# Performance work log

Hardware: AMD Instinct MI355X
Metric: run time of the kernel (lower is better)

Reference implementation:

```python
import jax, jax.numpy as jnp
import numpy as np

ND, NL, E, M = 8000, 16000, 60000, 50000  # disease nodes, lncrna nodes, edges, label edges
H = 16  # attention heads


def _gat(h_src, h_dst, src, dst, Ws, Wd, a_s, a_d, b, n_dst):
    # PyG GATConv: bipartite, concat heads, add_self_loops=False, negative_slope=0.2
    Hh, C = a_s.shape
    zs = (h_src @ Ws).reshape(-1, Hh, C)   # [Ns,H,C]
    zd = (h_dst @ Wd).reshape(-1, Hh, C)   # [Nd,H,C]
    al = (zs * a_s).sum(-1)[src] + (zd * a_d).sum(-1)[dst]  # [E,H]
    al = jax.nn.leaky_relu(al, negative_slope=0.2)
    m = jax.ops.segment_max(al, dst, num_segments=n_dst)
    m = jnp.where(jnp.isfinite(m), m, 0.0)  # guard empty segments
    e = jnp.exp(al - m[dst])
    s = jax.ops.segment_sum(e, dst, num_segments=n_dst)
    alpha = e / (s[dst] + 1e-16)            # softmax over incoming edges per dst
    msg = zs[src] * alpha[:, :, None]       # [E,H,C]
    out = jax.ops.segment_sum(msg, dst, num_segments=n_dst)
    return out.reshape(n_dst, Hh * C) + b


def _head_mean(x):
    x = jax.nn.relu(x)
    return x.reshape(x.shape[0], H, -1).mean(axis=1)


def _forward(x_d, x_l, emb_d, emb_l, lin_dw, lin_db, lin_lw, lin_lb,
             Wsrc1, Wdst1, asrc1, adst1, b1,
             Wsrc2, Wdst2, asrc2, adst2, b2,
             Wsrc3, Wdst3, asrc3, adst3, b3,
             pw, pb, fc1w, fc1b, fc2w, fc2b,
             node_id_d, node_id_l, edge_src, edge_dst, label_src, label_dst):
    hd = x_d @ lin_dw + lin_db + emb_d[node_id_d]   # [ND,128]
    hl = x_l @ lin_lw + lin_lb + emb_l[node_id_l]   # [NL,128]
    for (Ws, Wd, a_s, a_d, b) in ((Wsrc1, Wdst1, asrc1, adst1, b1),
                                  (Wsrc2, Wdst2, asrc2, adst2, b2),
                                  (Wsrc3, Wdst3, asrc3, adst3, b3)):
        # to_hetero: edge-type 0 = disease->lncrna (target lncrna); 1 = reverse
        out_l = _gat(hd, hl, edge_src, edge_dst, Ws[0], Wd[0], a_s[0], a_d[0], b[0], NL)
        out_d = _gat(hl, hd, edge_dst, edge_src, Ws[1], Wd[1], a_s[1], a_d[1], b[1], ND)
        hd, hl = _head_mean(out_d), _head_mean(out_l)
    # penalty scaling (per node type after to_hetero); transformer branch is dead code
    hd = hd * jnp.exp(hd @ pw[0] + pb[0])
    hl = hl * jnp.exp(hl @ pw[1] + pb[1])
    f = jnp.concatenate([hd[label_src], hl[label_dst]], axis=-1)  # [M,64]
    return jax.nn.relu(f @ fc1w + fc1b) @ fc2w + fc2b              # [M,1]


def setup_inputs():
    key = jax.random.key(0)
    ks = jax.random.split(key, 40)
    def rn(i, shape, scale=1.0):
        return jax.random.normal(ks[i], shape, dtype=jnp.float32) * scale
    return dict(
        x_d=rn(0, (ND, 412)), x_l=rn(1, (NL, 240)),
        node_id_d=jnp.arange(ND), node_id_l=jnp.arange(NL),
        edge_src=jax.random.randint(ks[2], (E,), 0, ND),
        edge_dst=jax.random.randint(ks[3], (E,), 0, NL),
        label_src=jax.random.randint(ks[4], (M,), 0, ND),
        label_dst=jax.random.randint(ks[5], (M,), 0, NL),
        emb_d=rn(6, (ND, 128), 0.1), emb_l=rn(7, (NL, 128), 0.1),
        lin_dw=rn(8, (412, 128), 412 ** -0.5), lin_db=rn(9, (128,), 0.02),
        lin_lw=rn(10, (240, 128), 240 ** -0.5), lin_lb=rn(11, (128,), 0.02),
        Wsrc1=rn(12, (2, 128, 2048), 128 ** -0.5), Wdst1=rn(13, (2, 128, 2048), 128 ** -0.5),
        asrc1=rn(14, (2, H, 128), 0.05), adst1=rn(15, (2, H, 128), 0.05), b1=rn(16, (2, 2048), 0.02),
        Wsrc2=rn(17, (2, 128, 2048), 128 ** -0.5), Wdst2=rn(18, (2, 128, 2048), 128 ** -0.5),
        asrc2=rn(19, (2, H, 128), 0.05), adst2=rn(20, (2, H, 128), 0.05), b2=rn(21, (2, 2048), 0.02),
        Wsrc3=rn(22, (2, 128, 512), 128 ** -0.5), Wdst3=rn(23, (2, 128, 512), 128 ** -0.5),
        asrc3=rn(24, (2, H, 32), 0.05), adst3=rn(25, (2, H, 32), 0.05), b3=rn(26, (2, 512), 0.02),
        pw=rn(27, (2, 32, 1), 0.05), pb=rn(28, (2, 1), 0.01),
        fc1w=rn(29, (64, 64), 64 ** -0.5), fc1b=rn(30, (64,), 0.02),
        fc2w=rn(31, (64, 1), 64 ** -0.5), fc2b=rn(32, (1,), 0.02),
    )


def reference(x_d, x_l, node_id_d, node_id_l, edge_src, edge_dst, label_src, label_dst,
              emb_d, emb_l, lin_dw, lin_db, lin_lw, lin_lb,
              Wsrc1, Wdst1, asrc1, adst1, b1,
              Wsrc2, Wdst2, asrc2, adst2, b2,
              Wsrc3, Wdst3, asrc3, adst3, b3,
              pw, pb, fc1w, fc1b, fc2w, fc2b):
    return _forward(x_d, x_l, emb_d, emb_l, lin_dw, lin_db, lin_lw, lin_lb,
                    Wsrc1, Wdst1, asrc1, adst1, b1,
                    Wsrc2, Wdst2, asrc2, adst2, b2,
                    Wsrc3, Wdst3, asrc3, adst3, b3,
                    pw, pb, fc1w, fc1b, fc2w, fc2b,
                    node_id_d, node_id_l, edge_src, edge_dst, label_src, label_dst)
```

## Files before the change

kernel.cpp:

```cpp
#include <hip/hip_runtime.h>
#include <cstdint>
#include <cstddef>

#define ND 8000
#define NL 16000
#define NE 60000
#define NM 50000

typedef __attribute__((ext_vector_type(8))) short bf16x8;
typedef __attribute__((ext_vector_type(4))) float f32x4;
typedef __attribute__((ext_vector_type(8))) unsigned int u32x8;

__device__ __forceinline__ unsigned short f2bf(float x) {
    unsigned int u = __float_as_uint(x);
    unsigned int r = (u + 0x7FFFu + ((u >> 16) & 1u)) >> 16;
    return (unsigned short)r;
}
__device__ __forceinline__ float bf2f(unsigned short b) {
    return __uint_as_float(((unsigned int)b) << 16);
}
__device__ __forceinline__ float lrelu(float x) {
    return x >= 0.f ? x : 0.2f * x;
}

__device__ __forceinline__ void gl_lds16(const void* g, void* l) {
    __builtin_amdgcn_global_load_lds(
        (const __attribute__((address_space(1))) void*)g,
        (__attribute__((address_space(3))) void*)l, 16, 0, 0);
}

__global__ void wtin_kernel(const float* __restrict__ Wd, const float* __restrict__ Wl,
                            unsigned short* __restrict__ WinH, unsigned short* __restrict__ WinL)
{
    int gid = blockIdx.x * 256 + threadIdx.x;
    if (gid >= 53248 + 32768) return;
    const float* W; int K, KC; unsigned short* oH; unsigned short* oL; int rem;
    if (gid < 53248) { W = Wd; K = 412; KC = 13; rem = gid; oH = WinH; oL = WinL; }
    else { W = Wl; K = 240; KC = 8; rem = gid - 53248; oH = WinH + 53248; oL = WinL + 53248; }
    int k = rem >> 7, n = rem & 127;
    float v = (k < K) ? W[(size_t)k * 128 + n] : 0.f;
    unsigned short hb = f2bf(v);
    unsigned short lb = f2bf(v - bf2f(hb));
    int u = n >> 4;
    int kc = k >> 5;
    int lane = (n & 15) + 16 * ((k >> 3) & 3);
    size_t o = ((size_t)u * KC + kc) * 512 + lane * 8 + (k & 7);
    oH[o] = hb;
    oL[o] = lb;
}

__global__ __launch_bounds__(256) void inlinm_kernel(
    const float* __restrict__ x_d, const float* __restrict__ x_l,
    const unsigned short* __restrict__ WinH, const unsigned short* __restrict__ WinL,
    const float* __restrict__ bd, const float* __restrict__ bl,
    const float* __restrict__ embd, const float* __restrict__ embl,
    const int* __restrict__ nidd, const int* __restrict__ nidl,
    float* __restrict__ hd, float* __restrict__ hl)
{
    const int tid = threadIdx.x;
    const int wave = tid >> 6;
    const int lane = tid & 63;
    const int i = blockIdx.x;
    const int cb = i & 1;
    int mt = i >> 1;
    const float* X; int K, KC;
    const unsigned short* wH; const unsigned short* wL;
    const float* bias; const float* emb; const int* nid; float* out;
    if (mt < 125) {
        X = x_d; K = 412; KC = 13; wH = WinH; wL = WinL;
        bias = bd; emb = embd; nid = nidd; out = hd;
    } else {
        mt -= 125;
        X = x_l; K = 240; KC = 8; wH = WinH + 53248; wL = WinL + 53248;
        bias = bl; emb = embl; nid = nidl; out = hl;
    }
    const int m0 = mt * 64 + wave * 16;
    const int row = lane & 15;
    const int quad = lane >> 4;

    f32x4 accH[4] = {};
    f32x4 accL[4] = {};

    const float* xr = X + (size_t)(m0 + row) * K;
    for (int kc = 0; kc < KC; ++kc) {
        int k0 = kc * 32 + quad * 8;
        float xv[8];
        if (k0 + 8 <= K) {
            float4 v0 = *(const float4*)(xr + k0);
            float4 v1 = *(const float4*)(xr + k0 + 4);
            xv[0] = v0.x; xv[1] = v0.y; xv[2] = v0.z; xv[3] = v0.w;
            xv[4] = v1.x; xv[5] = v1.y; xv[6] = v1.z; xv[7] = v1.w;
        } else {
#pragma unroll
            for (int j = 0; j < 8; ++j)
                xv[j] = (k0 + j < K) ? xr[k0 + j] : 0.f;
        }
        bf16x8 aH, aL;
#pragma unroll
        for (int j = 0; j < 8; ++j) {
            unsigned short hb = f2bf(xv[j]);
            aH[j] = (short)hb;
            aL[j] = (short)f2bf(xv[j] - bf2f(hb));
        }
#pragma unroll
        for (int u = 0; u < 4; ++u) {
            int ug = cb * 4 + u;
            size_t boff = ((size_t)ug * KC + kc) * 512 + lane * 8;
            bf16x8 bH = *(const bf16x8*)(wH + boff);
            bf16x8 bL = *(const bf16x8*)(wL + boff);
            accH[u] = __builtin_amdgcn_mfma_f32_16x16x32_bf16(aH, bH, accH[u], 0, 0, 0);
            accL[u] = __builtin_amdgcn_mfma_f32_16x16x32_bf16(aH, bL, accL[u], 0, 0, 0);
            accL[u] = __builtin_amdgcn_mfma_f32_16x16x32_bf16(aL, bH, accL[u], 0, 0, 0);
        }
    }
#pragma unroll
    for (int r = 0; r < 4; ++r) {
        int gm = m0 + quad * 4 + r;
        const float* ep = emb + (size_t)nid[gm] * 128;
        float* op = out + (size_t)gm * 128;
#pragma unroll
        for (int u = 0; u < 4; ++u) {
            int gn = (cb * 4 + u) * 16 + row;
            op[gn] = accH[u][r] + accL[u][r] + bias[gn] + ep[gn];
        }
    }
}

__global__ void wt2_kernel(const float* __restrict__ W0, const float* __restrict__ W1,
                           unsigned short* __restrict__ WtH, unsigned short* __restrict__ WtL)
{
    int gid = blockIdx.x * 256 + threadIdx.x;
    if (gid >= 2 * 2 * 128 * 2048) return;
    int l = gid >> 19;
    int rem0 = gid & 524287;
    int dir = rem0 >> 18;
    int rem = rem0 & 262143;
    int k = rem >> 11, n = rem & 2047;
    const float* W = l ? W1 : W0;
    float v = W[(size_t)dir * 262144 + (size_t)k * 2048 + n];
    unsigned short hb = f2bf(v);
    unsigned short lb = f2bf(v - bf2f(hb));
    int u = n >> 4;
    int lane = (n & 15) + 16 * ((k >> 3) & 3);
    size_t o = (size_t)l * 524288 + (size_t)dir * 262144 +
               ((size_t)u * 4 + (k >> 5)) * 512 + lane * 8 + (k & 7);
    WtH[o] = hb;
    WtL[o] = lb;
}

__global__ void wt3_kernel(const float* __restrict__ W3,
                           unsigned short* __restrict__ WtH3, unsigned short* __restrict__ WtL3)
{
    int gid = blockIdx.x * 256 + threadIdx.x;
    if (gid >= 2 * 128 * 512) return;
    int dir = gid >> 16;
    int rem = gid & 65535;
    int k = rem >> 9, n = rem & 511;
    float v = W3[(size_t)dir * 65536 + (size_t)k * 512 + n];
    unsigned short hb = f2bf(v);
    unsigned short lb = f2bf(v - bf2f(hb));
    int u = n >> 4;
    int lane = (n & 15) + 16 * ((k >> 3) & 3);
    size_t o = (size_t)dir * 65536 + ((size_t)u * 4 + (k >> 5)) * 512 + lane * 8 + (k & 7);
    WtH3[o] = hb;
    WtL3[o] = lb;
}

__global__ void pack3_kernel(const float* __restrict__ hd, const float* __restrict__ hl,
                             unsigned int* __restrict__ pAd, unsigned int* __restrict__ pAl)
{
    int gid = blockIdx.x * 256 + threadIdx.x;
    if (gid >= (ND + NL) * 128) return;
    int row = gid >> 7, k = gid & 127;
    const float* src; unsigned int* dst; int gm;
    if (row < ND) { src = hd; dst = pAd; gm = row; }
    else { src = hl; dst = pAl; gm = row - ND; }
    float v = src[(size_t)gm * 128 + k];
    unsigned short hb = f2bf(v);
    unsigned short lb = f2bf(v - bf2f(hb));
    int t = gm >> 4;
    int lane8 = ((gm & 15) + 16 * ((k >> 3) & 3)) * 8 + (k & 7);
    size_t idx = ((size_t)t * 4 + (k >> 5)) * 512 + lane8;
    dst[idx] = (unsigned int)hb | ((unsigned int)lb << 16);
}

__global__ __launch_bounds__(256) void gemm3m_kernel(
    const unsigned int* __restrict__ pAd, const unsigned int* __restrict__ pAl,
    const unsigned short* __restrict__ WtH3, const unsigned short* __restrict__ WtL3,
    float* __restrict__ zs3d, float* __restrict__ zs3l)
{
    const int tid = threadIdx.x;
    const int wave = tid >> 6;
    const int lane = tid & 63;
    const int cb = blockIdx.x & 1;
    int mt = blockIdx.x >> 1;
    const unsigned int* pA_; const unsigned short* wH; const unsigned short* wL; float* zs;
    if (mt < 125) { pA_ = pAd; wH = WtH3; wL = WtL3; zs = zs3d; }
    else { mt -= 125; pA_ = pAl; wH = WtH3 + 65536; wL = WtL3 + 65536; zs = zs3l; }
    const int m0 = mt * 64 + wave * 16;
    const int t = m0 >> 4;
    const int row = lane & 15;
    const int quad = lane >> 4;

    bf16x8 aH[4], aL[4];
#pragma unroll
    for (int kc = 0; kc < 4; ++kc) {
        u32x8 p = *(const u32x8*)(pA_ + ((size_t)t * 4 + kc) * 512 + lane * 8);
#pragma unroll
        for (int ii = 0; ii < 8; ++ii) {
            aH[kc][ii] = (short)(p[ii] & 0xffffu);
            aL[kc][ii] = (short)(p[ii] >> 16);
        }
    }

#pragma unroll 2
    for (int u = 0; u < 16; ++u) {
        const int ug = cb * 16 + u;
        f32x4 accH = (f32x4){0.f, 0.f, 0.f, 0.f};
        f32x4 accL = (f32x4){0.f, 0.f, 0.f, 0.f};
#pragma unroll
        for (int kc = 0; kc < 4; ++kc) {
            size_t boff = ((size_t)ug * 4 + kc) * 512 + lane * 8;
            bf16x8 bH = *(const bf16x8*)(wH + boff);
            bf16x8 bL = *(const bf16x8*)(wL + boff);
            accH = __builtin_amdgcn_mfma_f32_16x16x32_bf16(aH[kc], bH, accH, 0, 0, 0);
            accL = __builtin_amdgcn_mfma_f32_16x16x32_bf16(aH[kc], bL, accL, 0, 0, 0);
            accL = __builtin_amdgcn_mfma_f32_16x16x32_bf16(aL[kc], bH, accL, 0, 0, 0);
        }
        const int gn = ug * 16 + row;
#pragma unroll
        for (int r = 0; r < 4; ++r) {
            int gm = m0 + quad * 4 + r;
            zs[(size_t)gm * 512 + gn] = accH[r] + accL[r];
        }
    }
}

__global__ __launch_bounds__(256) void gemm2r_kernel(
    const unsigned int* __restrict__ haggPl, const unsigned int* __restrict__ haggPd,
    const unsigned short* __restrict__ WtHb, const unsigned short* __restrict__ WtLb,
    const float* __restrict__ biasb, float* __restrict__ outl, float* __restrict__ outd)
{
    __shared__ unsigned short BsH[2][4096];
    __shared__ unsigned short BsL[2][4096];

    const int tid = threadIdx.x;
    const int wave = tid >> 6;
    const int lane = tid & 63;
    const int bid = blockIdx.x;

    const unsigned int* haggP; const unsigned short* wHb; const unsigned short* wLb;
    const float* bias; float* out;
    int mt, cb, nmt;
    if (bid < 1024) {
        int g = bid & 7, rest = bid >> 3;
        mt = (rest >> 2) * 8 + g; cb = rest & 3; nmt = 250;
        haggP = haggPl; wHb = WtHb; wLb = WtLb; bias = biasb; out = outl;
    } else {
        int b2 = bid - 1024;
        int g = b2 & 7, rest = b2 >> 3;
        mt = (rest >> 2) * 8 + g; cb = rest & 3; nmt = 125;
        haggP = haggPd; wHb = WtHb + 262144; wLb = WtLb + 262144;
        bias = biasb + 2048; out = outd;
    }
    if (mt >= nmt) return;

    const int m0 = mt * 64 + wave * 16;
    const int t = m0 >> 4;
    const int row = lane & 15;
    const int quad = lane >> 4;

    const unsigned short* gHb = wHb + (size_t)cb * 4096;
    const unsigned short* gLb = wLb + (size_t)cb * 4096;

    u32x8 pA[4];
    f32x4 mean[2] = {};

#pragma unroll
    for (int j = 0; j < 2; ++j) {
        int o = (tid + j * 256) * 16;
        gl_lds16((const char*)gHb + o, (char*)&BsH[0][0] + o);
        gl_lds16((const char*)gLb + o, (char*)&BsL[0][0] + o);
    }
#pragma unroll
    for (int kc = 0; kc < 4; ++kc)
        pA[kc] = *(const u32x8*)(haggP + (((size_t)t * 16 + 0) * 4 + kc) * 512 + lane * 8);
    __syncthreads();

    int buf = 0;
    for (int h = 0; h < 16; ++h) {
        bf16x8 aH[4], aL[4];
#pragma unroll
        for (int kc = 0; kc < 4; ++kc) {
#pragma unroll
            for (int ii = 0; ii < 8; ++ii) {
                aH[kc][ii] = (short)(pA[kc][ii] & 0xffffu);
                aL[kc][ii] = (short)(pA[kc][ii] >> 16);
            }
        }
        if (h < 15) {
            const char* gH = (const char*)(gHb + (size_t)(h + 1) * 16384);
            const char* gL = (const char*)(gLb + (size_t)(h + 1) * 16384);
            char* lH = (char*)&BsH[buf ^ 1][0];
            char* lL = (char*)&BsL[buf ^ 1][0];
#pragma unroll
            for (int j = 0; j < 2; ++j) {
                int o = (tid + j * 256) * 16;
                gl_lds16(gH + o, lH + o);
                gl_lds16(gL + o, lL + o);
            }
#pragma unroll
            for (int kc = 0; kc < 4; ++kc)
                pA[kc] = *(const u32x8*)(haggP + (((size_t)t * 16 + h + 1) * 4 + kc) * 512 + lane * 8);
        }

#pragma unroll
        for (int ctl = 0; ctl < 2; ++ctl) {
            float bv = bias[h * 128 + cb * 32 + ctl * 16 + row];
            f32x4 accH = (f32x4){bv, bv, bv, bv};
            f32x4 accL = (f32x4){0.f, 0.f, 0.f, 0.f};
#pragma unroll
            for (int kc = 0; kc < 4; ++kc) {
                bf16x8 bH = *(const bf16x8*)&BsH[buf][(ctl * 4 + kc) * 512 + lane * 8];
                bf16x8 bL = *(const bf16x8*)&BsL[buf][(ctl * 4 + kc) * 512 + lane * 8];
                accH = __builtin_amdgcn_mfma_f32_16x16x32_bf16(aH[kc], bH, accH, 0, 0, 0);
                accL = __builtin_amdgcn_mfma_f32_16x16x32_bf16(aH[kc], bL, accL, 0, 0, 0);
                accL = __builtin_amdgcn_mfma_f32_16x16x32_bf16(aL[kc], bH, accL, 0, 0, 0);
            }
#pragma unroll
            for (int r = 0; r < 4; ++r)
                mean[ctl][r] += fmaxf(accH[r] + accL[r], 0.f);
        }
        __syncthreads();
        buf ^= 1;
    }

#pragma unroll
    for (int ctl = 0; ctl < 2; ++ctl) {
        int c = cb * 32 + ctl * 16 + row;
#pragma unroll
        for (int r = 0; r < 4; ++r) {
            int gm = m0 + quad * 4 + r;
            out[(size_t)gm * 128 + c] = mean[ctl][r] * (1.f / 16.f);
        }
    }
}

__global__ void fold3_kernel(
    const float* __restrict__ Ws1, const float* __restrict__ Wd1,
    const float* __restrict__ as1, const float* __restrict__ ad1,
    const float* __restrict__ Ws2, const float* __restrict__ Wd2,
    const float* __restrict__ as2, const float* __restrict__ ad2,
    const float* __restrict__ Ws3, const float* __restrict__ Wd3,
    const float* __restrict__ as3, const float* __restrict__ ad3,
    float* __restrict__ fw3)
{
    int gid = blockIdx.x * blockDim.x + threadIdx.x;
    if (gid >= 3 * 4 * 128 * 16) return;
    int l = gid / 8192, rem1 = gid % 8192;
    int f = rem1 / 2048, rem = rem1 % 2048;
    int k = rem >> 4, h = rem & 15;
    int Ntot = (l == 2) ? 512 : 2048;
    int C = Ntot >> 4;
    const float* W;
    const float* a;
    if (l == 0) { W = (f & 1) ? Wd1 : Ws1; a = (f & 1) ? ad1 : as1; }
    else if (l == 1) { W = (f & 1) ? Wd2 : Ws2; a = (f & 1) ? ad2 : as2; }
    else { W = (f & 1) ? Wd3 : Ws3; a = (f & 1) ? ad3 : as3; }
    if (f >= 2) { W += 128 * Ntot; a += 16 * C; }
    float s = 0.f;
    for (int c = 0; c < C; ++c) s += W[(size_t)k * Ntot + h * C + c] * a[h * C + c];
    fw3[gid] = s;
}

__global__ __launch_bounds__(256) void score2both_kernel(
    const float* __restrict__ Hd, const float* __restrict__ Hl,
    const float* __restrict__ fw,
    float* __restrict__ ssb0, float* __restrict__ sdb1,
    float* __restrict__ sdb0, float* __restrict__ ssb1)
{
    __shared__ float hs[16 * 128];
    __shared__ float wa[128 * 16];
    __shared__ float wb[128 * 16];
    int b = blockIdx.x;
    const float* Hf; const float* WfA; const float* WfB;
    float* outA; float* outB; int n0;
    if (b < ND / 16) {
        Hf = Hd; WfA = fw; WfB = fw + 3 * 2048; outA = ssb0; outB = sdb1; n0 = b * 16;
    } else {
        Hf = Hl; WfA = fw + 1 * 2048; WfB = fw + 2 * 2048; outA = sdb0; outB = ssb1;
        n0 = (b - ND / 16) * 16;
    }
    int tid = threadIdx.x;
#pragma unroll
    for (int i = 0; i < 8; ++i) {
        int idx = tid + i * 256;
        int nl = idx >> 7, k = idx & 127;
        hs[idx] = Hf[(size_t)(n0 + nl) * 128 + k];
        wa[idx] = WfA[idx];
        wb[idx] = WfB[idx];
    }
    __syncthreads();
    int nl = tid >> 4, h = tid & 15;
    float sa = 0.f, sb = 0.f;
    for (int k = 0; k < 128; ++k) {
        float hv = hs[nl * 128 + k];
        sa += hv * wa[k * 16 + h];
        sb += hv * wb[k * 16 + h];
    }
    int gn = n0 + nl;
    outA[gn * 16 + h] = sa;
    outB[gn * 16 + h] = sb;
}

__global__ void ms_kernel(
    const int* __restrict__ esrc, const int* __restrict__ edst,
    const float* __restrict__ ssb0, const float* __restrict__ sdb0,
    const float* __restrict__ ssb1, const float* __restrict__ sdb1,
    const int* __restrict__ offl, const int* __restrict__ csrl, float* __restrict__ msl,
    const int* __restrict__ offd, const int* __restrict__ csrd, float* __restrict__ msd)
{
    int t = blockIdx.x * 256 + threadIdx.x;
    const int* off; const int* csr; const int* srcidx;
    const float* ss; float sdv; float* ms; int d, h;
    if (t < NL * 16) {
        d = t >> 4; h = t & 15;
        off = offl; csr = csrl; srcidx = esrc; ss = ssb0;
        sdv = sdb0[d * 16 + h]; ms = msl;
    } else {
        t -= NL * 16;
        if (t >= ND * 16) return;
        d = t >> 4; h = t & 15;
        off = offd; csr = csrd; srcidx = edst; ss = ssb1;
        sdv = sdb1[d * 16 + h]; ms = msd;
    }
    int e0 = off[d], e1 = off[d + 1];
    float m = -1e30f, s = 0.f;
    for (int e = e0; e < e1; ++e) {
        int sn = srcidx[csr[e]];
        float a = lrelu(ss[sn * 16 + h] + sdv);
        if (a > m) { s = s * __expf(m - a) + 1.f; m = a; }
        else s += __expf(a - m);
    }
    ms[d * 32 + h] = m;
    ms[d * 32 + 16 + h] = s + 1e-16f;
}

__global__ void hist_kernel(const int* __restrict__ esrc, const int* __restrict__ edst,
                            int* __restrict__ degl, int* __restrict__ degd)
{
    int e = blockIdx.x * blockDim.x + threadIdx.x;
    if (e >= NE) return;
    atomicAdd(&degl[edst[e]], 1);
    atomicAdd(&degd[esrc[e]], 1);
}

__global__ __launch_bounds__(1024) void scan2_kernel(
    const int* __restrict__ degA, int* __restrict__ offA, int nA,
    const int* __restrict__ degB, int* __restrict__ offB, int nB)
{
    __shared__ int ps[1024];
    const int* deg = blockIdx.x ? degB : degA;
    int* off = blockIdx.x ? offB : offA;
    int n = blockIdx.x ? nB : nA;
    int tid = threadIdx.x;
    int chunk = (n + 1023) >> 10;
    int start = tid * chunk, end = min(start + chunk, n);
    int p = 0;
    for (int i = start; i < end; ++i) p += deg[i];
    ps[tid] = p;
    __syncthreads();
    for (int o = 1; o < 1024; o <<= 1) {
        int v = (tid >= o) ? ps[tid - o] : 0;
        __syncthreads();
        ps[tid] += v;
        __syncthreads();
    }
    int run = ps[tid] - p;
    for (int i = start; i < end; ++i) { off[i] = run; run += deg[i]; }
    if (tid == 1023) off[n] = ps[1023];
}

__global__ void scatter_kernel(const int* __restrict__ esrc, const int* __restrict__ edst,
                               const int* __restrict__ offl, const int* __restrict__ offd,
                               int* __restrict__ curl, int* __restrict__ curd,
                               int* __restrict__ csrl, int* __restrict__ csrd)
{
    int e = blockIdx.x * blockDim.x + threadIdx.x;
    if (e >= NE) return;
    int dl = edst[e]; int p = atomicAdd(&curl[dl], 1); csrl[offl[dl] + p] = e;
    int dd = esrc[e]; int q = atomicAdd(&curd[dd], 1); csrd[offd[dd] + q] = e;
}

__global__ __launch_bounds__(256) void hagg2_kernel(
    const float* __restrict__ hd, const float* __restrict__ hl,
    const float* __restrict__ ssb0, const float* __restrict__ sdb0, const float* __restrict__ msl,
    const float* __restrict__ ssb1, const float* __restrict__ sdb1, const float* __restrict__ msd,
    const int* __restrict__ offl, const int* __restrict__ csrl,
    const int* __restrict__ offd, const int* __restrict__ csrd,
    const int* __restrict__ esrc, const int* __restrict__ edst,
    unsigned int* __restrict__ haggPl, unsigned int* __restrict__ haggPd)
{
    __shared__ float alpha_s[2][8][17];
    __shared__ int src_s[2][8];
    const int b = blockIdx.x;
    const int tid = threadIdx.x;

    const float* hsrc; const float* ss; const float* sd; const float* ms;
    const int* off; const int* csr; const int* srcidx; unsigned int* haggP;
    int d0;
    if (b < NL / 2) {
        d0 = b * 2;
        hsrc = hd; ss = ssb0; sd = sdb0; ms = msl;
        off = offl; csr = csrl; srcidx = esrc; haggP = haggPl;
    } else {
        d0 = (b - NL / 2) * 2;
        hsrc = hl; ss = ssb1; sd = sdb1; ms = msd;
        off = offd; csr = csrd; srcidx = edst; haggP = haggPd;
    }

    const int half = tid >> 7;
    const int c = tid & 127;
    const int d = d0 + half;
    const int my_e0 = off[d];
    const int my_deg = off[d + 1] - my_e0;
    const int deg0 = off[d0 + 1] - off[d0];
    const int deg1 = off[d0 + 2] - off[d0 + 1];
    const int degmax = deg0 > deg1 ? deg0 : deg1;
    const int ntrip = (degmax + 7) >> 3;

    float acc[16];
#pragma unroll
    for (int h = 0; h < 16; ++h) acc[h] = 0.f;

    for (int trip = 0; trip < ntrip; ++trip) {
        int ce = trip * 8;
        {
            int ei = c >> 4, h = c & 15;
            if (ce + ei < my_deg) {
                int eid = csr[my_e0 + ce + ei];
                int sn = srcidx[eid];
                float a = lrelu(ss[sn * 16 + h] + sd[d * 16 + h]);
                alpha_s[half][ei][h] = __expf(a - ms[d * 32 + h]) / ms[d * 32 + 16 + h];
                if (h == 0) src_s[half][ei] = sn;
            }
        }
        __syncthreads();
        int nc = min(8, my_deg - ce);
        for (int ei = 0; ei < nc; ++ei) {
            float v = hsrc[(size_t)src_s[half][ei] * 128 + c];
#pragma unroll
            for (int h = 0; h < 16; ++h)
                acc[h] += alpha_s[half][ei][h] * v;
        }
        __syncthreads();
    }

    const int t = d >> 4;
    const int lane8 = ((d & 15) + 16 * ((c >> 3) & 3)) * 8 + (c & 7);
    const int kc = c >> 5;
#pragma unroll
    for (int h = 0; h < 16; ++h) {
        float v = acc[h];
        unsigned short hb = f2bf(v);
        unsigned short lb = f2bf(v - bf2f(hb));
        size_t idx = (((size_t)t * 16 + h) * 4 + kc) * 512 + lane8;
        haggP[idx] = (unsigned int)hb | ((unsigned int)lb << 16);
    }
}

__global__ __launch_bounds__(256) void agg32both_kernel(
    const float* __restrict__ zs3d, const float* __restrict__ zs3l,
    const float* __restrict__ ssb0, const float* __restrict__ sdb0, const float* __restrict__ msl,
    const float* __restrict__ ssb1, const float* __restrict__ sdb1, const float* __restrict__ msd,
    const int* __restrict__ offl, const int* __restrict__ csrl,
    const int* __restrict__ offd, const int* __restrict__ csrd,
    const int* __restrict__ esrc, const int* __restrict__ edst,
    const float* __restrict__ bias512,
    const float* __restrict__ pw, const float* __restrict__ pb,
    float* __restrict__ hlp, float* __restrict__ hdp)
{
    int d = blockIdx.x * 4 + (threadIdx.x >> 6);
    if (d >= NL + ND) return;
    const int lane = threadIdx.x & 63;

    const float* zs; const float* ss; const float* sd; const float* ms;
    const int* off; const int* csr; const int* srcidx;
    const float* bias; const float* pwt; const float* pbt; float* out;
    if (d < NL) {
        zs = zs3d; ss = ssb0; sd = sdb0; ms = msl;
        off = offl; csr = csrl; srcidx = esrc;
        bias = bias512; pwt = pw + 32; pbt = pb + 1; out = hlp;
    } else {
        d -= NL;
        zs = zs3l; ss = ssb1; sd = sdb1; ms = msd;
        off = offd; csr = csrd; srcidx = edst;
        bias = bias512 + 512; pwt = pw; pbt = pb; out = hdp;
    }

    const int h = lane >> 2;
    const int c0 = lane * 8;

    const float sdv = sd[d * 16 + h];
    const float mh = ms[d * 32 + h];
    const float sh = ms[d * 32 + 16 + h];
    const int e0 = off[d], e1 = off[d + 1];

    float acc[8] = {};
    for (int e = e0; e < e1; ++e) {
        int sn = srcidx[csr[e]];
        float a = lrelu(ss[sn * 16 + h] + sdv);
        float alpha = __expf(a - mh) / sh;
        const float* zr = zs + (size_t)sn * 512 + c0;
        float4 v0 = *(const float4*)zr;
        float4 v1 = *(const float4*)(zr + 4);
        acc[0] += alpha * v0.x; acc[1] += alpha * v0.y;
        acc[2] += alpha * v0.z; acc[3] += alpha * v0.w;
        acc[4] += alpha * v1.x; acc[5] += alpha * v1.y;
        acc[6] += alpha * v1.z; acc[7] += alpha * v1.w;
    }

#pragma unroll
    for (int i = 0; i < 8; ++i)
        acc[i] = fmaxf(acc[i] + bias[c0 + i], 0.f);

#pragma unroll
    for (int m = 4; m <= 32; m <<= 1)
#pragma unroll
        for (int i = 0; i < 8; ++i)
            acc[i] += __shfl_xor(acc[i], m);

    float hr[8];
#pragma unroll
    for (int i = 0; i < 8; ++i) hr[i] = acc[i] * (1.f / 16.f);

    float p = 0.f;
    const int ko = (lane & 3) * 8;
#pragma unroll
    for (int i = 0; i < 8; ++i) p += hr[i] * pwt[ko + i];
    p += __shfl_xor(p, 1);
    p += __shfl_xor(p, 2);
    float t = expf(p + pbt[0]);

    if (lane < 4) {
        float* op = out + (size_t)d * 32 + lane * 8;
#pragma unroll
        for (int i = 0; i < 8; ++i) op[i] = hr[i] * t;
    }
}

__global__ __launch_bounds__(256) void mlp_kernel(
    const float* __restrict__ hd, const float* __restrict__ hl,
    const int* __restrict__ ls, const int* __restrict__ ld,
    const float* __restrict__ w1, const float* __restrict__ b1,
    const float* __restrict__ w2, const float* __restrict__ b2,
    float* __restrict__ out, int M)
{
    __shared__ float w1s[64 * 64];
    __shared__ float b1s[64];
    __shared__ float w2s[64];
    int tid = threadIdx.x;
#pragma unroll
    for (int i = 0; i < 16; ++i) w1s[tid + i * 256] = w1[tid + i * 256];
    if (tid < 64) { b1s[tid] = b1[tid]; w2s[tid] = w2[tid]; }
    __syncthreads();
    int m = blockIdx.x * 256 + tid;
    if (m >= M) return;
    float f[64];
    const float* hp = hd + (size_t)ls[m] * 32;
    const float* lp = hl + (size_t)ld[m] * 32;
#pragma unroll
    for (int c = 0; c < 32; ++c) { f[c] = hp[c]; f[32 + c] = lp[c]; }
    float o = b2[0];
    for (int j = 0; j < 64; ++j) {
        float hj = b1s[j];
#pragma unroll
        for (int k = 0; k < 64; ++k) hj += f[k] * w1s[k * 64 + j];
        hj = fmaxf(hj, 0.f);
        o += hj * w2s[j];
    }
    out[m] = o;
}

extern "C" void kernel_launch(void* const* d_in, const int* in_sizes, int n_in,
                              void* d_out, int out_size, void* d_ws, size_t ws_size,
                              hipStream_t stream)
{
    const float* x_d = (const float*)d_in[0];
    const float* x_l = (const float*)d_in[1];
    const int* node_id_d = (const int*)d_in[2];
    const int* node_id_l = (const int*)d_in[3];
    const int* edge_src = (const int*)d_in[4];
    const int* edge_dst = (const int*)d_in[5];
    const int* label_src = (const int*)d_in[6];
    const int* label_dst = (const int*)d_in[7];
    const float* emb_d = (const float*)d_in[8];
    const float* emb_l = (const float*)d_in[9];
    const float* lin_dw = (const float*)d_in[10];
    const float* lin_db = (const float*)d_in[11];
    const float* lin_lw = (const float*)d_in[12];
    const float* lin_lb = (const float*)d_in[13];
    const float* Ws[3] = {(const float*)d_in[14], (const float*)d_in[19], (const float*)d_in[24]};
    const float* Wd[3] = {(const float*)d_in[15], (const float*)d_in[20], (const float*)d_in[25]};
    const float* as_[3] = {(const float*)d_in[16], (const float*)d_in[21], (const float*)d_in[26]};
    const float* ad_[3] = {(const float*)d_in[17], (const float*)d_in[22], (const float*)d_in[27]};
    const float* bb[3] = {(const float*)d_in[18], (const float*)d_in[23], (const float*)d_in[28]};
    const float* pw = (const float*)d_in[29];
    const float* pb = (const float*)d_in[30];
    const float* fc1w = (const float*)d_in[31];
    const float* fc1b = (const float*)d_in[32];
    const float* fc2w = (const float*)d_in[33];
    const float* fc2b = (const float*)d_in[34];

    char* wsb = (char*)d_ws;
    size_t woff = 0;
    auto carve = [&](size_t bytes) -> void* {
        woff = (woff + 255) & ~(size_t)255;
        void* p = wsb + woff;
        woff += bytes;
        return p;
    };
    float* hdA = (float*)carve((size_t)ND * 128 * 4);
    float* hlA = (float*)carve((size_t)NL * 128 * 4);
    float* hdB = (float*)carve((size_t)ND * 128 * 4);
    float* hlB = (float*)carve((size_t)NL * 128 * 4);
    unsigned int* haggPl = (unsigned int*)carve((size_t)NL * 2048 * 4);
    unsigned int* haggPd = (unsigned int*)carve((size_t)ND * 2048 * 4);
    unsigned short* WtH = (unsigned short*)carve((size_t)2 * 2 * 2048 * 128 * 2);
    unsigned short* WtL = (unsigned short*)carve((size_t)2 * 2 * 2048 * 128 * 2);
    unsigned short* WtH3 = (unsigned short*)carve((size_t)2 * 128 * 512 * 2);
    unsigned short* WtL3 = (unsigned short*)carve((size_t)2 * 128 * 512 * 2);
    unsigned short* WtInH = (unsigned short*)carve((size_t)(53248 + 32768) * 2);
    unsigned short* WtInL = (unsigned short*)carve((size_t)(53248 + 32768) * 2);
    unsigned int* pAd = (unsigned int*)carve((size_t)(ND / 16) * 4 * 512 * 4);
    unsigned int* pAl = (unsigned int*)carve((size_t)(NL / 16) * 4 * 512 * 4);
    float* ssb0 = (float*)carve((size_t)ND * 16 * 4);
    float* sdb0 = (float*)carve((size_t)NL * 16 * 4);
    float* ssb1 = (float*)carve((size_t)NL * 16 * 4);
    float* sdb1 = (float*)carve((size_t)ND * 16 * 4);
    float* msl = (float*)carve((size_t)NL * 32 * 4);
    float* msd = (float*)carve((size_t)ND * 32 * 4);
    float* fw3 = (float*)carve((size_t)3 * 4 * 2048 * 4);
    int* degl = (int*)carve((size_t)(2 * (NL + ND)) * 4);
    int* degd = degl + NL;
    int* curl = degd + ND;
    int* curd = curl + NL;
    int* offl = (int*)carve((size_t)(NL + 1) * 4);
    int* offd = (int*)carve((size_t)(ND + 1) * 4);
    int* csrl = (int*)carve((size_t)NE * 4);
    int* csrd = (int*)carve((size_t)NE * 4);
    float* hdp = (float*)carve((size_t)ND * 32 * 4);
    float* hlp = (float*)carve((size_t)NL * 32 * 4);

    hipMemsetAsync(degl, 0, (size_t)2 * (NL + ND) * 4, stream);

    hist_kernel<<<(NE + 255) / 256, 256, 0, stream>>>(edge_src, edge_dst, degl, degd);
    scan2_kernel<<<2, 1024, 0, stream>>>(degl, offl, NL, degd, offd, ND);
    scatter_kernel<<<(NE + 255) / 256, 256, 0, stream>>>(edge_src, edge_dst, offl, offd, curl, curd, csrl, csrd);

    fold3_kernel<<<(3 * 8192 + 255) / 256, 256, 0, stream>>>(
        Ws[0], Wd[0], as_[0], ad_[0], Ws[1], Wd[1], as_[1], ad_[1],
        Ws[2], Wd[2], as_[2], ad_[2], fw3);
    wt2_kernel<<<(2 * 524288 + 255) / 256, 256, 0, stream>>>(Ws[0], Ws[1], WtH, WtL);
    wt3_kernel<<<(2 * 65536 + 255) / 256, 256, 0, stream>>>(Ws[2], WtH3, WtL3);
    wtin_kernel<<<(53248 + 32768 + 255) / 256, 256, 0, stream>>>(lin_dw, lin_lw, WtInH, WtInL);

    inlinm_kernel<<<(125 + 250) * 2, 256, 0, stream>>>(
        x_d, x_l, WtInH, WtInL, lin_db, lin_lb, emb_d, emb_l,
        node_id_d, node_id_l, hdA, hlA);

    float* hd_cur = hdA; float* hd_nxt = hdB;
    float* hl_cur = hlA; float* hl_nxt = hlB;

    const int grid_ms = ((NL + ND) * 16 + 255) / 256;

    for (int L = 0; L < 2; ++L) {
        const float* fw = fw3 + (size_t)L * 8192;
        const unsigned short* wtH = WtH + (size_t)L * 524288;
        const unsigned short* wtL = WtL + (size_t)L * 524288;

        score2both_kernel<<<ND / 16 + NL / 16, 256, 0, stream>>>(
            hd_cur, hl_cur, fw, ssb0, sdb1, sdb0, ssb1);
        ms_kernel<<<grid_ms, 256, 0, stream>>>(edge_src, edge_dst, ssb0, sdb0, ssb1, sdb1,
                                               offl, csrl, msl, offd, csrd, msd);

        hagg2_kernel<<<NL / 2 + ND / 2, 256, 0, stream>>>(
            hd_cur, hl_cur, ssb0, sdb0, msl, ssb1, sdb1, msd,
            offl, csrl, offd, csrd, edge_src, edge_dst, haggPl, haggPd);

        gemm2r_kernel<<<1536, 256, 0, stream>>>(
            haggPl, haggPd, wtH, wtL, bb[L], hl_nxt, hd_nxt);

        float* t;
        t = hd_cur; hd_cur = hd_nxt; hd_nxt = t;
        t = hl_cur; hl_cur = hl_nxt; hl_nxt = t;
    }

    {
        const float* fw = fw3 + 2 * 8192;
        float* zs3d = (float*)haggPl;
        float* zs3l = (float*)haggPl + (size_t)ND * 512;
        score2both_kernel<<<ND / 16 + NL / 16, 256, 0, stream>>>(
            hd_cur, hl_cur, fw, ssb0, sdb1, sdb0, ssb1);
        ms_kernel<<<grid_ms, 256, 0, stream>>>(edge_src, edge_dst, ssb0, sdb0, ssb1, sdb1,
                                               offl, csrl, msl, offd, csrd, msd);

        pack3_kernel<<<((ND + NL) * 128 + 255) / 256, 256, 0, stream>>>(
            hd_cur, hl_cur, pAd, pAl);
        gemm3m_kernel<<<(125 + 250) * 2, 256, 0, stream>>>(
            pAd, pAl, WtH3, WtL3, zs3d, zs3l);

        agg32both_kernel<<<(NL + ND + 3) / 4, 256, 0, stream>>>(
            zs3d, zs3l, ssb0, sdb0, msl, ssb1, sdb1, msd,
            offl, csrl, offd, csrd, edge_src, edge_dst,
            bb[2], pw, pb, hlp, hdp);
    }

    mlp_kernel<<<(NM + 255) / 256, 256, 0, stream>>>(hdp, hlp, label_src, label_dst,
                                                     fc1w, fc1b, fc2w, fc2b, (float*)d_out, NM);
}
```

Before: 636.5 us.

## Restructure gemm2r to stage activations in LDS and stream weights from global

Result: no change. 625.8 us, median of 2 (-1.7%).

```diff
diff --git a/kernel.cpp b/kernel.cpp
--- a/kernel.cpp
+++ b/kernel.cpp
@@ -241,8 +241,7 @@
     const unsigned short* __restrict__ WtHb, const unsigned short* __restrict__ WtLb,
     const float* __restrict__ biasb, float* __restrict__ outl, float* __restrict__ outd)
 {
-    __shared__ unsigned short BsH[2][4096];
-    __shared__ unsigned short BsL[2][4096];
+    __shared__ unsigned int As[2][4096];
 
     const int tid = threadIdx.x;
     const int wave = tid >> 6;
@@ -250,100 +249,93 @@
     const int bid = blockIdx.x;
 
     const unsigned int* haggP; const unsigned short* wHb; const unsigned short* wLb;
-    const float* bias; float* out;
-    int mt, cb, nmt;
-    if (bid < 1024) {
-        int g = bid & 7, rest = bid >> 3;
-        mt = (rest >> 2) * 8 + g; cb = rest & 3; nmt = 250;
-        haggP = haggPl; wHb = WtHb; wLb = WtLb; bias = biasb; out = outl;
+    const float* bias; float* out; int mt;
+    if (bid < 500) {
+        mt = bid; haggP = haggPl; wHb = WtHb; wLb = WtLb; bias = biasb; out = outl;
     } else {
-        int b2 = bid - 1024;
-        int g = b2 & 7, rest = b2 >> 3;
-        mt = (rest >> 2) * 8 + g; cb = rest & 3; nmt = 125;
-        haggP = haggPd; wHb = WtHb + 262144; wLb = WtLb + 262144;
+        mt = bid - 500; haggP = haggPd; wHb = WtHb + 262144; wLb = WtLb + 262144;
         bias = biasb + 2048; out = outd;
     }
-    if (mt >= nmt) return;
-
-    const int m0 = mt * 64 + wave * 16;
-    const int t = m0 >> 4;
+    const int cb = wave;
+    const int t0 = mt * 2;
     const int row = lane & 15;
     const int quad = lane >> 4;
 
-    const unsigned short* gHb = wHb + (size_t)cb * 4096;
-    const unsigned short* gLb = wLb + (size_t)cb * 4096;
-
-    u32x8 pA[4];
-    f32x4 mean[2] = {};
-
-#pragma unroll
-    for (int j = 0; j < 2; ++j) {
-        int o = (tid + j * 256) * 16;
-        gl_lds16((const char*)gHb + o, (char*)&BsH[0][0] + o);
-        gl_lds16((const char*)gLb + o, (char*)&BsL[0][0] + o);
-    }
-#pragma unroll
-    for (int kc = 0; kc < 4; ++kc)
-        pA[kc] = *(const u32x8*)(haggP + (((size_t)t * 16 + 0) * 4 + kc) * 512 + lane * 8);
+    auto stageA = [&](int h, int b) {
+#pragma unroll
+        for (int j = 0; j < 4; ++j) {
+            int slot = tid + j * 256;
+            int t = slot >> 9;
+            const char* g = (const char*)(haggP + ((size_t)(t0 + t) * 16 + h) * 2048)
+                            + (size_t)(slot & 511) * 16;
+            char* l = (char*)&As[b][0] + (size_t)slot * 16;
+            gl_lds16(g, l);
+        }
+    };
+
+    f32x4 mean[2][2] = {};
+
+    stageA(0, 0);
     __syncthreads();
 
     int buf = 0;
     for (int h = 0; h < 16; ++h) {
-        bf16x8 aH[4], aL[4];
-#pragma unroll
-        for (int kc = 0; kc < 4; ++kc) {
-#pragma unroll
-            for (int ii = 0; ii < 8; ++ii) {
-                aH[kc][ii] = (short)(pA[kc][ii] & 0xffffu);
-                aL[kc][ii] = (short)(pA[kc][ii] >> 16);
+        if (h < 15) stageA(h + 1, buf ^ 1);
+
+        bf16x8 aH[2][4], aL[2][4];
+#pragma unroll
+        for (int t = 0; t < 2; ++t)
+#pragma unroll
+            for (int kc = 0; kc < 4; ++kc) {
+                u32x8 p = *(const u32x8*)&As[buf][t * 2048 + kc * 512 + lane * 8];
+#pragma unroll
+                for (int ii = 0; ii < 8; ++ii) {
+                    aH[t][kc][ii] = (short)(p[ii] & 0xffffu);
+                    aL[t][kc][ii] = (short)(p[ii] >> 16);
+                }
             }
-        }
-        if (h < 15) {
-            const char* gH = (const char*)(gHb + (size_t)(h + 1) * 16384);
-            const char* gL = (const char*)(gLb + (size_t)(h + 1) * 16384);
-            char* lH = (char*)&BsH[buf ^ 1][0];
-            char* lL = (char*)&BsL[buf ^ 1][0];
-#pragma unroll
-            for (int j = 0; j < 2; ++j) {
-                int o = (tid + j * 256) * 16;
-                gl_lds16(gH + o, lH + o);
-                gl_lds16(gL + o, lL + o);
+
+#pragma unroll
+        for (int ctl = 0; ctl < 2; ++ctl) {
+            const int u = h * 8 + cb * 2 + ctl;
+            float bv = bias[h * 128 + cb * 32 + ctl * 16 + row];
+            f32x4 accH0 = (f32x4){bv, bv, bv, bv};
+            f32x4 accL0 = (f32x4){0.f, 0.f, 0.f, 0.f};
+            f32x4 accH1 = (f32x4){bv, bv, bv, bv};
+            f32x4 accL1 = (f32x4){0.f, 0.f, 0.f, 0.f};
+#pragma unroll
+            for (int kc = 0; kc < 4; ++kc) {
+                size_t boff = ((size_t)u * 4 + kc) * 512 + lane * 8;
+                bf16x8 bH = *(const bf16x8*)(wHb + boff);
+                bf16x8 bL = *(const bf16x8*)(wLb + boff);
+                accH0 = __builtin_amdgcn_mfma_f32_16x16x32_bf16(aH[0][kc], bH, accH0, 0, 0, 0);
+                accL0 = __builtin_amdgcn_mfma_f32_16x16x32_bf16(aH[0][kc], bL, accL0, 0, 0, 0);
+                accL0 = __builtin_amdgcn_mfma_f32_16x16x32_bf16(aL[0][kc], bH, accL0, 0, 0, 0);
+                accH1 = __builtin_amdgcn_mfma_f32_16x16x32_bf16(aH[1][kc], bH, accH1, 0, 0, 0);
+                accL1 = __builtin_amdgcn_mfma_f32_16x16x32_bf16(aH[1][kc], bL, accL1, 0, 0, 0);
+                accL1 = __builtin_amdgcn_mfma_f32_16x16x32_bf16(aL[1][kc], bH, accL1, 0, 0, 0);
             }
 #pragma unroll
-            for (int kc = 0; kc < 4; ++kc)
-                pA[kc] = *(const u32x8*)(haggP + (((size_t)t * 16 + h + 1) * 4 + kc) * 512 + lane * 8);
-        }
-
-#pragma unroll
-        for (int ctl = 0; ctl < 2; ++ctl) {
-            float bv = bias[h * 128 + cb * 32 + ctl * 16 + row];
-            f32x4 accH = (f32x4){bv, bv, bv, bv};
-            f32x4 accL = (f32x4){0.f, 0.f, 0.f, 0.f};
-#pragma unroll
-            for (int kc = 0; kc < 4; ++kc) {
-                bf16x8 bH = *(const bf16x8*)&BsH[buf][(ctl * 4 + kc) * 512 + lane * 8];
-                bf16x8 bL = *(const bf16x8*)&BsL[buf][(ctl * 4 + kc) * 512 + lane * 8];
-                accH = __builtin_amdgcn_mfma_f32_16x16x32_bf16(aH[kc], bH, accH, 0, 0, 0);
-                accL = __builtin_amdgcn_mfma_f32_16x16x32_bf16(aH[kc], bL, accL, 0, 0, 0);
-                accL = __builtin_amdgcn_mfma_f32_16x16x32_bf16(aL[kc], bH, accL, 0, 0, 0);
+            for (int r = 0; r < 4; ++r) {
+                mean[0][ctl][r] += fmaxf(accH0[r] + accL0[r], 0.f);
+                mean[1][ctl][r] += fmaxf(accH1[r] + accL1[r], 0.f);
             }
-#pragma unroll
-            for (int r = 0; r < 4; ++r)
-                mean[ctl][r] += fmaxf(accH[r] + accL[r], 0.f);
         }
         __syncthreads();
         buf ^= 1;
     }
 
 #pragma unroll
-    for (int ctl = 0; ctl < 2; ++ctl) {
-        int c = cb * 32 + ctl * 16 + row;
-#pragma unroll
-        for (int r = 0; r < 4; ++r) {
-            int gm = m0 + quad * 4 + r;
-            out[(size_t)gm * 128 + c] = mean[ctl][r] * (1.f / 16.f);
-        }
-    }
+    for (int t = 0; t < 2; ++t)
+#pragma unroll
+        for (int ctl = 0; ctl < 2; ++ctl) {
+            int c = cb * 32 + ctl * 16 + row;
+#pragma unroll
+            for (int r = 0; r < 4; ++r) {
+                int gm = mt * 32 + t * 16 + quad * 4 + r;
+                out[(size_t)gm * 128 + c] = mean[t][ctl][r] * (1.f / 16.f);
+            }
+        }
 }
 
 __global__ void fold3_kernel(
@@ -788,7 +780,7 @@
             hd_cur, hl_cur, ssb0, sdb0, msl, ssb1, sdb1, msd,
             offl, csrl, offd, csrd, edge_src, edge_dst, haggPl, haggPd);
 
-        gemm2r_kernel<<<1536, 256, 0, stream>>>(
+        gemm2r_kernel<<<500 + 250, 256, 0, stream>>>(
             haggPl, haggPd, wtH, wtL, bb[L], hl_nxt, hd_nxt);
 
         float* t;
```

## Drop LDS staging in gemm2r; each wave computes independent 16-row by 64-col tile

Applied to the files above, without the earlier changes.

Measured after the change: 669.7 us. 5.2% more time.

```diff
diff --git a/kernel.cpp b/kernel.cpp
--- a/kernel.cpp
+++ b/kernel.cpp
@@ -21,12 +21,6 @@
 }
 __device__ __forceinline__ float lrelu(float x) {
     return x >= 0.f ? x : 0.2f * x;
-}
-
-__device__ __forceinline__ void gl_lds16(const void* g, void* l) {
-    __builtin_amdgcn_global_load_lds(
-        (const __attribute__((address_space(1))) void*)g,
-        (__attribute__((address_space(3))) void*)l, 16, 0, 0);
 }
 
 __global__ void wtin_kernel(const float* __restrict__ Wd, const float* __restrict__ Wl,
@@ -241,53 +235,32 @@
     const unsigned short* __restrict__ WtHb, const unsigned short* __restrict__ WtLb,
     const float* __restrict__ biasb, float* __restrict__ outl, float* __restrict__ outd)
 {
-    __shared__ unsigned short BsH[2][4096];
-    __shared__ unsigned short BsL[2][4096];
-
     const int tid = threadIdx.x;
     const int wave = tid >> 6;
     const int lane = tid & 63;
-    const int bid = blockIdx.x;
+    int item = blockIdx.x * 4 + wave;
 
     const unsigned int* haggP; const unsigned short* wHb; const unsigned short* wLb;
-    const float* bias; float* out;
-    int mt, cb, nmt;
-    if (bid < 1024) {
-        int g = bid & 7, rest = bid >> 3;
-        mt = (rest >> 2) * 8 + g; cb = rest & 3; nmt = 250;
+    const float* bias; float* out; int t, cb;
+    if (item < 2000) {
+        t = item >> 1; cb = item & 1;
         haggP = haggPl; wHb = WtHb; wLb = WtLb; bias = biasb; out = outl;
     } else {
-        int b2 = bid - 1024;
-        int g = b2 & 7, rest = b2 >> 3;
-        mt = (rest >> 2) * 8 + g; cb = rest & 3; nmt = 125;
+        item -= 2000;
+        t = item >> 1; cb = item & 1;
         haggP = haggPd; wHb = WtHb + 262144; wLb = WtLb + 262144;
         bias = biasb + 2048; out = outd;
     }
-    if (mt >= nmt) return;
-
-    const int m0 = mt * 64 + wave * 16;
-    const int t = m0 >> 4;
     const int row = lane & 15;
     const int quad = lane >> 4;
 
-    const unsigned short* gHb = wHb + (size_t)cb * 4096;
-    const unsigned short* gLb = wLb + (size_t)cb * 4096;
-
     u32x8 pA[4];
-    f32x4 mean[2] = {};
-
-#pragma unroll
-    for (int j = 0; j < 2; ++j) {
-        int o = (tid + j * 256) * 16;
-        gl_lds16((const char*)gHb + o, (char*)&BsH[0][0] + o);
-        gl_lds16((const char*)gLb + o, (char*)&BsL[0][0] + o);
-    }
 #pragma unroll
     for (int kc = 0; kc < 4; ++kc)
         pA[kc] = *(const u32x8*)(haggP + (((size_t)t * 16 + 0) * 4 + kc) * 512 + lane * 8);
-    __syncthreads();
-
-    int buf = 0;
+
+    f32x4 mean[4] = {};
+
     for (int h = 0; h < 16; ++h) {
         bf16x8 aH[4], aL[4];
 #pragma unroll
@@ -299,30 +272,22 @@
             }
         }
         if (h < 15) {
-            const char* gH = (const char*)(gHb + (size_t)(h + 1) * 16384);
-            const char* gL = (const char*)(gLb + (size_t)(h + 1) * 16384);
-            char* lH = (char*)&BsH[buf ^ 1][0];
-            char* lL = (char*)&BsL[buf ^ 1][0];
-#pragma unroll
-            for (int j = 0; j < 2; ++j) {
-                int o = (tid + j * 256) * 16;
-                gl_lds16(gH + o, lH + o);
-                gl_lds16(gL + o, lL + o);
-            }
 #pragma unroll
             for (int kc = 0; kc < 4; ++kc)
                 pA[kc] = *(const u32x8*)(haggP + (((size_t)t * 16 + h + 1) * 4 + kc) * 512 + lane * 8);
         }
 
 #pragma unroll
-        for (int ctl = 0; ctl < 2; ++ctl) {
-            float bv = bias[h * 128 + cb * 32 + ctl * 16 + row];
+        for (int ctl = 0; ctl < 4; ++ctl) {
+            const int u = h * 8 + cb * 4 + ctl;
+            float bv = bias[h * 128 + cb * 64 + ctl * 16 + row];
             f32x4 accH = (f32x4){bv, bv, bv, bv};
             f32x4 accL = (f32x4){0.f, 0.f, 0.f, 0.f};
 #pragma unroll
             for (int kc = 0; kc < 4; ++kc) {
-                bf16x8 bH = *(const bf16x8*)&BsH[buf][(ctl * 4 + kc) * 512 + lane * 8];
-                bf16x8 bL = *(const bf16x8*)&BsL[buf][(ctl * 4 + kc) * 512 + lane * 8];
+                size_t boff = ((size_t)u * 4 + kc) * 512 + lane * 8;
+                bf16x8 bH = *(const bf16x8*)(wHb + boff);
+                bf16x8 bL = *(const bf16x8*)(wLb + boff);
                 accH = __builtin_amdgcn_mfma_f32_16x16x32_bf16(aH[kc], bH, accH, 0, 0, 0);
                 accL = __builtin_amdgcn_mfma_f32_16x16x32_bf16(aH[kc], bL, accL, 0, 0, 0);
                 accL = __builtin_amdgcn_mfma_f32_16x16x32_bf16(aL[kc], bH, accL, 0, 0, 0);
@@ -331,16 +296,14 @@
             for (int r = 0; r < 4; ++r)
                 mean[ctl][r] += fmaxf(accH[r] + accL[r], 0.f);
         }
-        __syncthreads();
-        buf ^= 1;
-    }
-
-#pragma unroll
-    for (int ctl = 0; ctl < 2; ++ctl) {
-        int c = cb * 32 + ctl * 16 + row;
+    }
+
+#pragma unroll
+    for (int ctl = 0; ctl < 4; ++ctl) {
+        int c = cb * 64 + ctl * 16 + row;
 #pragma unroll
         for (int r = 0; r < 4; ++r) {
-            int gm = m0 + quad * 4 + r;
+            int gm = t * 16 + quad * 4 + r;
             out[(size_t)gm * 128 + c] = mean[ctl][r] * (1.f / 16.f);
         }
     }
@@ -788,7 +751,7 @@
             hd_cur, hl_cur, ssb0, sdb0, msl, ssb1, sdb1, msd,
             offl, csrl, offd, csrd, edge_src, edge_dst, haggPl, haggPd);
 
-        gemm2r_kernel<<<1536, 256, 0, stream>>>(
+        gemm2r_kernel<<<750, 256, 0, stream>>>(
             haggPl, haggPd, wtH, wtL, bb[L], hl_nxt, hd_nxt);
 
         float* t;
```
